# Kernel optimization log

Measured on AMD Instinct MI355X. Metric: run time of the kernel, lower is better.

## Reference

```python
import jax, jax.numpy as jnp
import numpy as np

B, N, NID, V, GH, PHI, RHO = 8, 256, 64, 128, 128, 256, 128
BN = B * N
EPS = 1e-5


def _layernorm(x, g, b):
    m = jnp.mean(x, axis=-1, keepdims=True)
    v = jnp.var(x, axis=-1, keepdims=True)
    return (x - m) * jax.lax.rsqrt(v + EPS) * g + b


def _edges(A):
    # dense adjacency -> flat batched edge list, exactly as mask.nonzero() ordering
    bidx = jnp.arange(B)[:, None, None]
    ii = jnp.arange(N)[None, :, None]
    jj = jnp.arange(N)[None, None, :]
    src = jnp.broadcast_to(bidx * N + ii, (B, N, N)).reshape(-1)  # edge_index[0] = b*N+i
    tgt = jnp.broadcast_to(bidx * N + jj, (B, N, N)).reshape(-1)  # edge_index[1] = b*N+j
    w = A.reshape(-1)
    valid = w != 0
    rel = (w > 0).astype(jnp.int32)
    return src, tgt, w, valid, rel


def _rgcn(H, src, tgt, valid, rel, Wrel, Wroot, bias):
    # torch_geometric RGCNConv: mean aggregation per relation at target + root + bias
    x_src = H[src]  # (E, d) gather
    out = H @ Wroot + bias
    for r in range(2):
        m = (valid & (rel == r)).astype(H.dtype)  # (E,)
        s = jax.ops.segment_sum(x_src * m[:, None], tgt, num_segments=BN)
        c = jax.ops.segment_sum(m, tgt, num_segments=BN)
        out = out + (s / jnp.maximum(c, 1.0)[:, None]) @ Wrel[r]
    return out


def setup_inputs() -> dict:
    key = jax.random.key(0)
    ks = jax.random.split(key, 24)
    p = lambda k, shape: jax.random.normal(k, shape, dtype=jnp.float32) * 0.02
    z = lambda *shape: jnp.zeros(shape, jnp.float32)
    return {
        "A": jax.random.normal(ks[0], (B, N, N), dtype=jnp.float32),
        "X": jax.random.normal(ks[1], (B, N, NID), dtype=jnp.float32),
        "home_mask": (jax.random.uniform(ks[2], (B, N)) > 0.5).astype(jnp.float32),
        "emb1_w": p(ks[3], (NID, V)), "emb1_b": z(V),
        "emb2_w": p(ks[4], (V, V)), "emb2_b": z(V),
        "rgcn_w_0": p(ks[5], (2, V, GH)), "rgcn_root_0": p(ks[6], (V, GH)), "rgcn_bias_0": z(GH),
        "lina_w_0": p(ks[7], (GH, GH)), "lina_b_0": z(GH),
        "linb_w_0": p(ks[8], (GH, GH)), "linb_b_0": z(GH),
        "rgcn_w_1": p(ks[9], (2, GH, GH)), "rgcn_root_1": p(ks[10], (GH, GH)), "rgcn_bias_1": z(GH),
        "lina_w_1": p(ks[11], (GH, GH)), "lina_b_1": z(GH),
        "linb_w_1": p(ks[12], (GH, GH)), "linb_b_1": z(GH),
        "norm_g": jnp.ones((GH,), jnp.float32), "norm_b": z(GH),
        "phi_w1": p(ks[13], (GH, PHI)), "phi_b1": z(PHI),
        "phi_w2": p(ks[14], (PHI, PHI)), "phi_b2": z(PHI),
        "rho_w1": p(ks[15], (PHI, RHO)), "rho_b1": z(RHO),
        "rho_w2": p(ks[16], (RHO, 1)), "rho_b2": z(1),
    }


def reference(A, X, home_mask, emb1_w, emb1_b, emb2_w, emb2_b,
              rgcn_w_0, rgcn_root_0, rgcn_bias_0, lina_w_0, lina_b_0, linb_w_0, linb_b_0,
              rgcn_w_1, rgcn_root_1, rgcn_bias_1, lina_w_1, lina_b_1, linb_w_1, linb_b_1,
              norm_g, norm_b, phi_w1, phi_b1, phi_w2, phi_b2,
              rho_w1, rho_b1, rho_w2, rho_b2):
    away_mask = 1.0 - home_mask
    H = jax.nn.relu(X @ emb1_w + emb1_b)
    H = (H @ emb2_w + emb2_b).reshape(BN, V)

    src, tgt, w, valid, rel = _edges(A)
    aw = jnp.abs(w) * valid.astype(w.dtype)  # |edge_weight|, zero for masked-out edges

    blocks = [
        (rgcn_w_0, rgcn_root_0, rgcn_bias_0, lina_w_0, lina_b_0, linb_w_0, linb_b_0),
        (rgcn_w_1, rgcn_root_1, rgcn_bias_1, lina_w_1, lina_b_1, linb_w_1, linb_b_1),
    ]
    agg = jnp.zeros_like(H)
    for (Wrel, Wroot, bias, law, lab, lbw, lbb) in blocks:
        H = H + agg
        H2 = _rgcn(H, src, tgt, valid, rel, Wrel, Wroot, bias)
        # gather-scale-scatter: agg[src] += H2[tgt] * |w|
        agg = jax.ops.segment_sum(H2[tgt] * aw[:, None], src, num_segments=BN)
        agg = jax.nn.relu(_layernorm(agg, norm_g, norm_b))  # dropout = identity (eval)
        agg = jax.nn.relu(agg @ law + lab)
        agg = agg @ lbw + lbb
    H = (H + agg).reshape(B, N, GH)

    # DeepSet phi (dropout = identity)
    h = jax.nn.relu(H @ phi_w1 + phi_b1)
    phi_out = jax.nn.relu(h @ phi_w2 + phi_b2)  # (B, N, PHI)

    home_sum = jnp.sum(phi_out * home_mask[:, :, None], axis=1)
    away_sum = jnp.sum(phi_out * away_mask[:, :, None], axis=1)

    def rho(s):
        return (jax.nn.relu(s @ rho_w1 + rho_b1) @ rho_w2 + rho_b2)[:, 0]

    out = rho(home_sum) - rho(away_sum)
    return 0.5 + 0.5 * jnp.tanh(out)  # (B,)
```

## Files before the change

kernel.cpp:

```cpp
#include <hip/hip_runtime.h>
#include <math.h>

#define NB 8

__global__ __launch_bounds__(512, 4) void k_embed(const float* __restrict__ X,
        const float* __restrict__ w1, const float* __restrict__ b1,
        const float* __restrict__ w2, const float* __restrict__ b2,
        float* __restrict__ H, float* __restrict__ pools) {
    const int r0 = blockIdx.x * 4;
    const int t = threadIdx.x, q = t & 31, u = t >> 5;
    __shared__ __align__(16) float part[8192];
    __shared__ __align__(16) float xq[256];
    __shared__ __align__(16) float h1q[512];
    if (blockIdx.x < 8) pools[blockIdx.x * 512 + t] = 0.f;
    if (t < 64) {
        float4 v;
        v.x = X[(size_t)(r0 + 0) * 64 + t];
        v.y = X[(size_t)(r0 + 1) * 64 + t];
        v.z = X[(size_t)(r0 + 2) * 64 + t];
        v.w = X[(size_t)(r0 + 3) * 64 + t];
        *(float4*)&xq[t * 4] = v;
    }
    __syncthreads();
    {
        float acc[16];
        #pragma unroll
        for (int i = 0; i < 16; ++i) acc[i] = 0.f;
        #pragma unroll
        for (int kk = 0; kk < 4; ++kk) {
            int k = u * 4 + kk;
            float4 w4 = *(const float4*)&w1[(size_t)k * 128 + q * 4];
            float wc[4] = {w4.x, w4.y, w4.z, w4.w};
            float4 x4 = *(const float4*)&xq[k * 4];
            float xr[4] = {x4.x, x4.y, x4.z, x4.w};
            #pragma unroll
            for (int r = 0; r < 4; ++r)
                #pragma unroll
                for (int c = 0; c < 4; ++c)
                    acc[r * 4 + c] = fmaf(xr[r], wc[c], acc[r * 4 + c]);
        }
        #pragma unroll
        for (int r = 0; r < 4; ++r)
            *(float4*)&part[u * 512 + r * 128 + q * 4] =
                make_float4(acc[r*4+0], acc[r*4+1], acc[r*4+2], acc[r*4+3]);
    }
    __syncthreads();
    {
        int r = t >> 7, f = t & 127;
        float s = b1[f];
        #pragma unroll
        for (int uu = 0; uu < 16; ++uu) s += part[uu * 512 + r * 128 + f];
        h1q[f * 4 + r] = fmaxf(s, 0.f);
    }
    __syncthreads();
    {
        float a2[16];
        #pragma unroll
        for (int i = 0; i < 16; ++i) a2[i] = 0.f;
        #pragma unroll
        for (int kk = 0; kk < 8; ++kk) {
            int k = u * 8 + kk;
            float4 w4 = *(const float4*)&w2[(size_t)k * 128 + q * 4];
            float wc[4] = {w4.x, w4.y, w4.z, w4.w};
            float4 h4 = *(const float4*)&h1q[k * 4];
            float hr[4] = {h4.x, h4.y, h4.z, h4.w};
            #pragma unroll
            for (int r = 0; r < 4; ++r)
                #pragma unroll
                for (int c = 0; c < 4; ++c)
                    a2[r * 4 + c] = fmaf(hr[r], wc[c], a2[r * 4 + c]);
        }
        #pragma unroll
        for (int r = 0; r < 4; ++r)
            *(float4*)&part[u * 512 + r * 128 + q * 4] =
                make_float4(a2[r*4+0], a2[r*4+1], a2[r*4+2], a2[r*4+3]);
    }
    __syncthreads();
    {
        int r = t >> 7, f = t & 127;
        float s = b2[f];
        #pragma unroll
        for (int uu = 0; uu < 16; ++uu) s += part[uu * 512 + r * 128 + f];
        H[(size_t)(r0 + r) * 128 + f] = s;
    }
}

__global__ __launch_bounds__(512, 4) void k_gcn1(
        const float* __restrict__ A, const float* __restrict__ H,
        const float* __restrict__ Wrel, const float* __restrict__ Wroot,
        const float* __restrict__ bias, float* __restrict__ H2) {
    const int b  = blockIdx.x >> 6;
    const int j0 = (blockIdx.x & 63) * 4;
    const int t = threadIdx.x, q = t & 31, u = t >> 5;
    __shared__ __align__(16) float maskM[2048];
    __shared__ __align__(16) float part[8192];
    __shared__ __align__(16) float pb[1536];
    __shared__ float cntp[256];
    __shared__ float cnt[8];
    const float* Ab = A + (size_t)b * 65536;
    const float* Hb = H + (size_t)b * 32768;
    const float* W0 = Wrel;
    const float* W1 = Wrel + 16384;

    if (t < 256) {
        float4 a = *(const float4*)(Ab + (size_t)t * 256 + j0);
        float4 m0, m1;
        m0.x = (a.x < 0.f) ? 1.f : 0.f; m1.x = (a.x > 0.f) ? 1.f : 0.f;
        m0.y = (a.y < 0.f) ? 1.f : 0.f; m1.y = (a.y > 0.f) ? 1.f : 0.f;
        m0.z = (a.z < 0.f) ? 1.f : 0.f; m1.z = (a.z > 0.f) ? 1.f : 0.f;
        m0.w = (a.w < 0.f) ? 1.f : 0.f; m1.w = (a.w > 0.f) ? 1.f : 0.f;
        *(float4*)&maskM[t * 8]     = m0;
        *(float4*)&maskM[t * 8 + 4] = m1;
    }
    __syncthreads();
    if (t < 256) {
        int chunk = t >> 3, slot = t & 7;
        float c = 0.f;
        #pragma unroll
        for (int qq = 0; qq < 8; ++qq) c += maskM[(chunk * 8 + qq) * 8 + slot];
        cntp[slot * 32 + chunk] = c;
    }
    float acc0[16], acc1[16];
    #pragma unroll
    for (int i = 0; i < 16; ++i) { acc0[i] = 0.f; acc1[i] = 0.f; }
    #pragma unroll 8
    for (int ii = 0; ii < 16; ++ii) {
        int i = u * 16 + ii;
        float4 h4 = *(const float4*)&Hb[(size_t)i * 128 + q * 4];
        float hc[4] = {h4.x, h4.y, h4.z, h4.w};
        float4 m0 = *(const float4*)&maskM[i * 8];
        float4 m1 = *(const float4*)&maskM[i * 8 + 4];
        float mr0[4] = {m0.x, m0.y, m0.z, m0.w};
        float mr1[4] = {m1.x, m1.y, m1.z, m1.w};
        #pragma unroll
        for (int r = 0; r < 4; ++r)
            #pragma unroll
            for (int c = 0; c < 4; ++c) {
                acc0[r * 4 + c] = fmaf(mr0[r], hc[c], acc0[r * 4 + c]);
                acc1[r * 4 + c] = fmaf(mr1[r], hc[c], acc1[r * 4 + c]);
            }
    }
    #pragma unroll
    for (int r = 0; r < 4; ++r)
        *(float4*)&part[u * 512 + r * 128 + q * 4] =
            make_float4(acc0[r*4+0], acc0[r*4+1], acc0[r*4+2], acc0[r*4+3]);
    if (t < 8) {
        float s = 0.f;
        #pragma unroll
        for (int c = 0; c < 32; ++c) s += cntp[t * 32 + c];
        cnt[t] = s;
    }
    __syncthreads();
    {
        int r = t >> 7, f = t & 127;
        float s = 0.f;
        #pragma unroll
        for (int uu = 0; uu < 16; ++uu) s += part[uu * 512 + r * 128 + f];
        pb[f * 12 + 4 + r] = s * (1.f / fmaxf(cnt[r], 1.f));
    }
    __syncthreads();
    #pragma unroll
    for (int r = 0; r < 4; ++r)
        *(float4*)&part[u * 512 + r * 128 + q * 4] =
            make_float4(acc1[r*4+0], acc1[r*4+1], acc1[r*4+2], acc1[r*4+3]);
    __syncthreads();
    {
        int r = t >> 7, f = t & 127;
        float s = 0.f;
        #pragma unroll
        for (int uu = 0; uu < 16; ++uu) s += part[uu * 512 + r * 128 + f];
        pb[f * 12 + 8 + r] = s * (1.f / fmaxf(cnt[4 + r], 1.f));
    }
    if (t < 128) {
        int r = t >> 5, fq = t & 31;
        float4 g4 = *(const float4*)(Hb + (size_t)(j0 + r) * 128 + fq * 4);
        pb[(fq * 4 + 0) * 12 + r] = g4.x;
        pb[(fq * 4 + 1) * 12 + r] = g4.y;
        pb[(fq * 4 + 2) * 12 + r] = g4.z;
        pb[(fq * 4 + 3) * 12 + r] = g4.w;
    }
    __syncthreads();
    float bcc[16];
    #pragma unroll
    for (int i = 0; i < 16; ++i) bcc[i] = 0.f;
    #pragma unroll 4
    for (int kk = 0; kk < 8; ++kk) {
        int k = u * 8 + kk;
        float4 wr = *(const float4*)&Wroot[(size_t)k * 128 + q * 4];
        float4 wa = *(const float4*)&W0[(size_t)k * 128 + q * 4];
        float4 wb = *(const float4*)&W1[(size_t)k * 128 + q * 4];
        float wrc[4] = {wr.x, wr.y, wr.z, wr.w};
        float wac[4] = {wa.x, wa.y, wa.z, wa.w};
        float wbc[4] = {wb.x, wb.y, wb.z, wb.w};
        float4 hv = *(const float4*)&pb[k * 12];
        float4 q0 = *(const float4*)&pb[k * 12 + 4];
        float4 q1 = *(const float4*)&pb[k * 12 + 8];
        float hr[4] = {hv.x, hv.y, hv.z, hv.w};
        float m0r[4] = {q0.x, q0.y, q0.z, q0.w};
        float m1r[4] = {q1.x, q1.y, q1.z, q1.w};
        #pragma unroll
        for (int r = 0; r < 4; ++r)
            #pragma unroll
            for (int c = 0; c < 4; ++c) {
                float v = bcc[r * 4 + c];
                v = fmaf(hr[r], wrc[c], v);
                v = fmaf(m0r[r], wac[c], v);
                v = fmaf(m1r[r], wbc[c], v);
                bcc[r * 4 + c] = v;
            }
    }
    #pragma unroll
    for (int r = 0; r < 4; ++r)
        *(float4*)&part[u * 512 + r * 128 + q * 4] =
            make_float4(bcc[r*4+0], bcc[r*4+1], bcc[r*4+2], bcc[r*4+3]);
    __syncthreads();
    {
        int r = t >> 7, f = t & 127;
        float s = bias[f];
        #pragma unroll
        for (int uu = 0; uu < 16; ++uu) s += part[uu * 512 + r * 128 + f];
        H2[(size_t)(b * 256 + j0 + r) * 128 + f] = s;
    }
}

__global__ __launch_bounds__(512, 4) void k_gcn2(
        const float* __restrict__ A, const float* __restrict__ H2,
        const float* __restrict__ g, const float* __restrict__ bta,
        const float* __restrict__ law, const float* __restrict__ lab,
        const float* __restrict__ lbw, const float* __restrict__ lbb,
        float* __restrict__ H) {
    const int b  = blockIdx.x >> 6;
    const int i0 = (blockIdx.x & 63) * 4;
    const int t = threadIdx.x, q = t & 31, u = t >> 5;
    __shared__ __align__(16) float part[8192];
    __shared__ __align__(16) float absA[1024];
    __shared__ __align__(16) float xq[512];
    __shared__ __align__(16) float uq[512];
    __shared__ float red[16];
    __shared__ float mi[8];
    const float* Ab  = A + (size_t)b * 65536;
    const float* H2b = H2 + (size_t)b * 32768;

    if (t < 256) {
        float4 av;
        av.x = fabsf(Ab[(size_t)(i0 + 0) * 256 + t]);
        av.y = fabsf(Ab[(size_t)(i0 + 1) * 256 + t]);
        av.z = fabsf(Ab[(size_t)(i0 + 2) * 256 + t]);
        av.w = fabsf(Ab[(size_t)(i0 + 3) * 256 + t]);
        *(float4*)&absA[t * 4] = av;
    }
    __syncthreads();
    float acc[16];
    #pragma unroll
    for (int i = 0; i < 16; ++i) acc[i] = 0.f;
    #pragma unroll 8
    for (int jj = 0; jj < 16; ++jj) {
        int j = u * 16 + jj;
        float4 h4 = *(const float4*)&H2b[(size_t)j * 128 + q * 4];
        float hc[4] = {h4.x, h4.y, h4.z, h4.w};
        float4 a4 = *(const float4*)&absA[j * 4];
        float ar[4] = {a4.x, a4.y, a4.z, a4.w};
        #pragma unroll
        for (int r = 0; r < 4; ++r)
            #pragma unroll
            for (int c = 0; c < 4; ++c)
                acc[r * 4 + c] = fmaf(ar[r], hc[c], acc[r * 4 + c]);
    }
    #pragma unroll
    for (int r = 0; r < 4; ++r)
        *(float4*)&part[u * 512 + r * 128 + q * 4] =
            make_float4(acc[r*4+0], acc[r*4+1], acc[r*4+2], acc[r*4+3]);
    __syncthreads();
    const int rr = t >> 7, ff = t & 127;
    float x;
    {
        float s = 0.f;
        #pragma unroll
        for (int uu = 0; uu < 16; ++uu) s += part[uu * 512 + rr * 128 + ff];
        x = s;
        float s2 = x * x;
        float sw = x;
        #pragma unroll
        for (int o = 32; o > 0; o >>= 1) {
            sw += __shfl_down(sw, o, 64);
            s2 += __shfl_down(s2, o, 64);
        }
        int w = (t >> 6) & 1;
        if ((t & 63) == 0) {
            red[(rr * 2 + w) * 2]     = sw;
            red[(rr * 2 + w) * 2 + 1] = s2;
        }
    }
    __syncthreads();
    if (t < 4) {
        float s  = red[t * 4]     + red[t * 4 + 2];
        float s2 = red[t * 4 + 1] + red[t * 4 + 3];
        float m = s * (1.f / 128.f);
        float v = s2 * (1.f / 128.f) - m * m;
        mi[t * 2] = m;
        mi[t * 2 + 1] = rsqrtf(v + 1e-5f);
    }
    __syncthreads();
    xq[ff * 4 + rr] = fmaxf((x - mi[rr * 2]) * mi[rr * 2 + 1] * g[ff] + bta[ff], 0.f);
    __syncthreads();
    float u1[16];
    #pragma unroll
    for (int i = 0; i < 16; ++i) u1[i] = 0.f;
    #pragma unroll
    for (int kk = 0; kk < 8; ++kk) {
        int k = u * 8 + kk;
        float4 w4 = *(const float4*)&law[(size_t)k * 128 + q * 4];
        float wc[4] = {w4.x, w4.y, w4.z, w4.w};
        float4 x4 = *(const float4*)&xq[k * 4];
        float xr[4] = {x4.x, x4.y, x4.z, x4.w};
        #pragma unroll
        for (int r = 0; r < 4; ++r)
            #pragma unroll
            for (int c = 0; c < 4; ++c)
                u1[r * 4 + c] = fmaf(xr[r], wc[c], u1[r * 4 + c]);
    }
    #pragma unroll
    for (int r = 0; r < 4; ++r)
        *(float4*)&part[u * 512 + r * 128 + q * 4] =
            make_float4(u1[r*4+0], u1[r*4+1], u1[r*4+2], u1[r*4+3]);
    __syncthreads();
    {
        float s = lab[ff];
        #pragma unroll
        for (int uu = 0; uu < 16; ++uu) s += part[uu * 512 + rr * 128 + ff];
        uq[ff * 4 + rr] = fmaxf(s, 0.f);
    }
    __syncthreads();
    float u2[16];
    #pragma unroll
    for (int i = 0; i < 16; ++i) u2[i] = 0.f;
    #pragma unroll
    for (int kk = 0; kk < 8; ++kk) {
        int k = u * 8 + kk;
        float4 w4 = *(const float4*)&lbw[(size_t)k * 128 + q * 4];
        float wc[4] = {w4.x, w4.y, w4.z, w4.w};
        float4 x4 = *(const float4*)&uq[k * 4];
        float xr[4] = {x4.x, x4.y, x4.z, x4.w};
        #pragma unroll
        for (int r = 0; r < 4; ++r)
            #pragma unroll
            for (int c = 0; c < 4; ++c)
                u2[r * 4 + c] = fmaf(xr[r], wc[c], u2[r * 4 + c]);
    }
    #pragma unroll
    for (int r = 0; r < 4; ++r)
        *(float4*)&part[u * 512 + r * 128 + q * 4] =
            make_float4(u2[r*4+0], u2[r*4+1], u2[r*4+2], u2[r*4+3]);
    __syncthreads();
    {
        float s = lbb[ff];
        #pragma unroll
        for (int uu = 0; uu < 16; ++uu) s += part[uu * 512 + rr * 128 + ff];
        size_t idx = (size_t)(b * 256 + i0 + rr) * 128 + ff;
        H[idx] = s + H[idx];
    }
}

__global__ __launch_bounds__(512, 4) void k_deepset(
        const float* __restrict__ H, const float* __restrict__ hm,
        const float* __restrict__ w1, const float* __restrict__ b1,
        const float* __restrict__ w2, const float* __restrict__ b2,
        float* __restrict__ hsum, float* __restrict__ asum) {
    const int r0 = blockIdx.x * 4;
    const int b  = blockIdx.x >> 6;
    const int t  = threadIdx.x, q = t & 63, u = t >> 6;
    __shared__ __align__(16) float part[8192];
    __shared__ __align__(16) float ph2[1024];
    __shared__ __align__(16) float hraw[512];
    __shared__ float hmv[4];
    if (t < 128) {
        float4 g4 = *(const float4*)&H[(size_t)r0 * 128 + t * 4];
        *(float4*)&hraw[t * 4] = g4;
    }
    if (t < 4) hmv[t] = hm[r0 + t];
    __syncthreads();
    float acc[16];
    #pragma unroll
    for (int i = 0; i < 16; ++i) acc[i] = 0.f;
    #pragma unroll 8
    for (int kk = 0; kk < 16; ++kk) {
        int k = u * 16 + kk;
        float4 w4 = *(const float4*)&w1[(size_t)k * 256 + q * 4];
        float wc[4] = {w4.x, w4.y, w4.z, w4.w};
        float hr[4];
        #pragma unroll
        for (int r = 0; r < 4; ++r) hr[r] = hraw[r * 128 + k];
        #pragma unroll
        for (int r = 0; r < 4; ++r)
            #pragma unroll
            for (int c = 0; c < 4; ++c)
                acc[r * 4 + c] = fmaf(hr[r], wc[c], acc[r * 4 + c]);
    }
    #pragma unroll
    for (int r = 0; r < 4; ++r)
        *(float4*)&part[u * 1024 + r * 256 + q * 4] =
            make_float4(acc[r*4+0], acc[r*4+1], acc[r*4+2], acc[r*4+3]);
    __syncthreads();
    {
        #pragma unroll
        for (int e = 0; e < 2; ++e) {
            int idx = e * 512 + t;
            int r = idx >> 8, f = idx & 255;
            float s = b1[f];
            #pragma unroll
            for (int uu = 0; uu < 8; ++uu) s += part[uu * 1024 + r * 256 + f];
            ph2[r * 256 + f] = fmaxf(s, 0.f);
        }
    }
    __syncthreads();
    float a2[16];
    #pragma unroll
    for (int i = 0; i < 16; ++i) a2[i] = 0.f;
    #pragma unroll 8
    for (int kk = 0; kk < 32; ++kk) {
        int k = u * 32 + kk;
        float4 w4 = *(const float4*)&w2[(size_t)k * 256 + q * 4];
        float wc[4] = {w4.x, w4.y, w4.z, w4.w};
        float pr[4];
        #pragma unroll
        for (int r = 0; r < 4; ++r) pr[r] = ph2[r * 256 + k];
        #pragma unroll
        for (int r = 0; r < 4; ++r)
            #pragma unroll
            for (int c = 0; c < 4; ++c)
                a2[r * 4 + c] = fmaf(pr[r], wc[c], a2[r * 4 + c]);
    }
    #pragma unroll
    for (int r = 0; r < 4; ++r)
        *(float4*)&part[u * 1024 + r * 256 + q * 4] =
            make_float4(a2[r*4+0], a2[r*4+1], a2[r*4+2], a2[r*4+3]);
    __syncthreads();
    if (t < 256) {
        float bb = b2[t];
        float hp = 0.f, sp = 0.f;
        #pragma unroll
        for (int r = 0; r < 4; ++r) {
            float s = bb;
            #pragma unroll
            for (int uu = 0; uu < 8; ++uu) s += part[uu * 1024 + r * 256 + t];
            float p = fmaxf(s, 0.f);
            sp += p;
            hp = fmaf(p, hmv[r], hp);
        }
        atomicAdd(&hsum[b * 256 + t], hp);
        atomicAdd(&asum[b * 256 + t], sp - hp);
    }
}

__global__ __launch_bounds__(256) void k_rho(const float* __restrict__ hsum,
        const float* __restrict__ asum,
        const float* __restrict__ w1, const float* __restrict__ b1,
        const float* __restrict__ w2, const float* __restrict__ b2,
        float* __restrict__ out) {
    const int bIdx = blockIdx.x;
    const int t = threadIdx.x, q = t & 31, u = t >> 5;
    __shared__ __align__(16) float part[2048];
    __shared__ __align__(16) float sv[512];
    __shared__ float wsv[2];
    sv[t] = hsum[bIdx * 256 + t];
    sv[256 + t] = asum[bIdx * 256 + t];
    __syncthreads();
    float aH[4] = {0.f, 0.f, 0.f, 0.f}, aA[4] = {0.f, 0.f, 0.f, 0.f};
    #pragma unroll 8
    for (int kk = 0; kk < 32; ++kk) {
        int k = u * 32 + kk;
        float4 w4 = *(const float4*)&w1[(size_t)k * 128 + q * 4];
        float sh = sv[k], sa = sv[256 + k];
        aH[0] = fmaf(sh, w4.x, aH[0]); aA[0] = fmaf(sa, w4.x, aA[0]);
        aH[1] = fmaf(sh, w4.y, aH[1]); aA[1] = fmaf(sa, w4.y, aA[1]);
        aH[2] = fmaf(sh, w4.z, aH[2]); aA[2] = fmaf(sa, w4.z, aA[2]);
        aH[3] = fmaf(sh, w4.w, aH[3]); aA[3] = fmaf(sa, w4.w, aA[3]);
    }
    *(float4*)&part[u * 256 + q * 4]       = make_float4(aH[0], aH[1], aH[2], aH[3]);
// ... 26 lines not shown
                              hipStream_t stream) {
    const float* A         = (const float*)d_in[0];
    const float* X         = (const float*)d_in[1];
    const float* home_mask = (const float*)d_in[2];
    const float* emb1_w    = (const float*)d_in[3];
    const float* emb1_b    = (const float*)d_in[4];
    const float* emb2_w    = (const float*)d_in[5];
    const float* emb2_b    = (const float*)d_in[6];
    const float* rgcn_w[2]    = { (const float*)d_in[7],  (const float*)d_in[14] };
    const float* rgcn_root[2] = { (const float*)d_in[8],  (const float*)d_in[15] };
    const float* rgcn_bias[2] = { (const float*)d_in[9],  (const float*)d_in[16] };
    const float* lina_w[2]    = { (const float*)d_in[10], (const float*)d_in[17] };
    const float* lina_b[2]    = { (const float*)d_in[11], (const float*)d_in[18] };
    const float* linb_w[2]    = { (const float*)d_in[12], (const float*)d_in[19] };
    const float* linb_b[2]    = { (const float*)d_in[13], (const float*)d_in[20] };
    const float* norm_g  = (const float*)d_in[21];
    const float* norm_b  = (const float*)d_in[22];
    const float* phi_w1  = (const float*)d_in[23];
    const float* phi_b1  = (const float*)d_in[24];
    const float* phi_w2  = (const float*)d_in[25];
    const float* phi_b2  = (const float*)d_in[26];
    const float* rho_w1  = (const float*)d_in[27];
    const float* rho_b1  = (const float*)d_in[28];
    const float* rho_w2  = (const float*)d_in[29];
    const float* rho_b2  = (const float*)d_in[30];
    float* out = (float*)d_out;

    float* ws   = (float*)d_ws;
    float* H    = ws;
    float* H2   = ws + 262144;
    float* hsum = ws + 524288;
    float* asum = ws + 526336;

    k_embed<<<512, 512, 0, stream>>>(X, emb1_w, emb1_b, emb2_w, emb2_b, H, hsum);

    for (int it = 0; it < 2; ++it) {
        k_gcn1<<<512, 512, 0, stream>>>(A, H, rgcn_w[it], rgcn_root[it],
                                        rgcn_bias[it], H2);
        k_gcn2<<<512, 512, 0, stream>>>(A, H2, norm_g, norm_b,
                                        lina_w[it], lina_b[it],
                                        linb_w[it], linb_b[it], H);
    }

    k_deepset<<<512, 512, 0, stream>>>(H, home_mask, phi_w1, phi_b1,
                                       phi_w2, phi_b2, hsum, asum);
    k_rho<<<NB, 256, 0, stream>>>(hsum, asum, rho_w1, rho_b1, rho_w2, rho_b2, out);
}
```

Before: 189.3 us.

## Process eight rows per block and pre-reduce partials with wave shuffles

Each block of the embed, GCN and DeepSet kernels now handles 8 output rows instead of 4, so every weight and H row loaded from global memory is reused across twice as many rows and the grids shrink from 512 to 256 blocks. Before each shared-memory reduction, the two half-waves of each 64-lane wave are combined with __shfl_down, so the shared partial buffer holds 8 slices instead of 16 and the final summation loop is shorter. The larger register tile (32 accumulators) and lower launch-bounds occupancy hint raise register pressure. With only 256 blocks the GPU may be underfilled, and the DeepSet kernel needs extra reduction passes and barriers.

Measured after the change: 206.5 us. +9.1%, slower.

```diff
diff --git a/kernel.cpp b/kernel.cpp
--- a/kernel.cpp
+++ b/kernel.cpp
@@ -3,296 +3,342 @@
 
 #define NB 8
 
-__global__ __launch_bounds__(512, 4) void k_embed(const float* __restrict__ X,
+
+__global__ __launch_bounds__(512, 2) void k_embed(const float* __restrict__ X,
         const float* __restrict__ w1, const float* __restrict__ b1,
         const float* __restrict__ w2, const float* __restrict__ b2,
         float* __restrict__ H, float* __restrict__ pools) {
-    const int r0 = blockIdx.x * 4;
-    const int t = threadIdx.x, q = t & 31, u = t >> 5;
+    const int r0 = blockIdx.x * 8;
+    const int t = threadIdx.x, q = t & 31, u = t >> 5, w = t >> 6;
     __shared__ __align__(16) float part[8192];
-    __shared__ __align__(16) float xq[256];
-    __shared__ __align__(16) float h1q[512];
+    __shared__ __align__(16) float xq[512];
+    __shared__ __align__(16) float h1q[1024];
     if (blockIdx.x < 8) pools[blockIdx.x * 512 + t] = 0.f;
-    if (t < 64) {
-        float4 v;
-        v.x = X[(size_t)(r0 + 0) * 64 + t];
-        v.y = X[(size_t)(r0 + 1) * 64 + t];
-        v.z = X[(size_t)(r0 + 2) * 64 + t];
-        v.w = X[(size_t)(r0 + 3) * 64 + t];
-        *(float4*)&xq[t * 4] = v;
-    }
-    __syncthreads();
-    {
-        float acc[16];
-        #pragma unroll
-        for (int i = 0; i < 16; ++i) acc[i] = 0.f;
+    {
+        int r = t >> 6, k = t & 63;
+        xq[k * 8 + r] = X[(size_t)(r0 + r) * 64 + k];
+    }
+    __syncthreads();
+    {
+        float acc[32];
+        #pragma unroll
+        for (int i = 0; i < 32; ++i) acc[i] = 0.f;
         #pragma unroll
         for (int kk = 0; kk < 4; ++kk) {
             int k = u * 4 + kk;
             float4 w4 = *(const float4*)&w1[(size_t)k * 128 + q * 4];
             float wc[4] = {w4.x, w4.y, w4.z, w4.w};
-            float4 x4 = *(const float4*)&xq[k * 4];
-            float xr[4] = {x4.x, x4.y, x4.z, x4.w};
-            #pragma unroll
-            for (int r = 0; r < 4; ++r)
+            float4 xa = *(const float4*)&xq[k * 8];
+            float4 xb = *(const float4*)&xq[k * 8 + 4];
+            float xr[8] = {xa.x, xa.y, xa.z, xa.w, xb.x, xb.y, xb.z, xb.w};
+            #pragma unroll
+            for (int r = 0; r < 8; ++r)
                 #pragma unroll
                 for (int c = 0; c < 4; ++c)
                     acc[r * 4 + c] = fmaf(xr[r], wc[c], acc[r * 4 + c]);
         }
         #pragma unroll
-        for (int r = 0; r < 4; ++r)
-            *(float4*)&part[u * 512 + r * 128 + q * 4] =
-                make_float4(acc[r*4+0], acc[r*4+1], acc[r*4+2], acc[r*4+3]);
-    }
-    __syncthreads();
-    {
-        int r = t >> 7, f = t & 127;
+        for (int i = 0; i < 32; ++i) acc[i] += __shfl_down(acc[i], 32, 64);
+        if ((t & 63) < 32)
+            #pragma unroll
+            for (int r = 0; r < 8; ++r)
+                *(float4*)&part[w * 1024 + r * 128 + q * 4] =
+                    make_float4(acc[r*4+0], acc[r*4+1], acc[r*4+2], acc[r*4+3]);
+    }
+    __syncthreads();
+    #pragma unroll
+    for (int e = 0; e < 2; ++e) {
+        int idx = e * 512 + t;
+        int r = idx >> 7, f = idx & 127;
         float s = b1[f];
         #pragma unroll
-        for (int uu = 0; uu < 16; ++uu) s += part[uu * 512 + r * 128 + f];
-        h1q[f * 4 + r] = fmaxf(s, 0.f);
-    }
-    __syncthreads();
-    {
-        float a2[16];
-        #pragma unroll
-        for (int i = 0; i < 16; ++i) a2[i] = 0.f;
+        for (int uu = 0; uu < 8; ++uu) s += part[uu * 1024 + r * 128 + f];
+        h1q[f * 8 + r] = fmaxf(s, 0.f);
+    }
+    __syncthreads();
+    {
+        float acc[32];
+        #pragma unroll
+        for (int i = 0; i < 32; ++i) acc[i] = 0.f;
         #pragma unroll
         for (int kk = 0; kk < 8; ++kk) {
             int k = u * 8 + kk;
             float4 w4 = *(const float4*)&w2[(size_t)k * 128 + q * 4];
             float wc[4] = {w4.x, w4.y, w4.z, w4.w};
-            float4 h4 = *(const float4*)&h1q[k * 4];
-            float hr[4] = {h4.x, h4.y, h4.z, h4.w};
-            #pragma unroll
-            for (int r = 0; r < 4; ++r)
+            float4 xa = *(const float4*)&h1q[k * 8];
+            float4 xb = *(const float4*)&h1q[k * 8 + 4];
+            float xr[8] = {xa.x, xa.y, xa.z, xa.w, xb.x, xb.y, xb.z, xb.w};
+            #pragma unroll
+            for (int r = 0; r < 8; ++r)
                 #pragma unroll
                 for (int c = 0; c < 4; ++c)
-                    a2[r * 4 + c] = fmaf(hr[r], wc[c], a2[r * 4 + c]);
-        }
-        #pragma unroll
-        for (int r = 0; r < 4; ++r)
-            *(float4*)&part[u * 512 + r * 128 + q * 4] =
-                make_float4(a2[r*4+0], a2[r*4+1], a2[r*4+2], a2[r*4+3]);
-    }
-    __syncthreads();
-    {
-        int r = t >> 7, f = t & 127;
+                    acc[r * 4 + c] = fmaf(xr[r], wc[c], acc[r * 4 + c]);
+        }
+        #pragma unroll
+        for (int i = 0; i < 32; ++i) acc[i] += __shfl_down(acc[i], 32, 64);
+        if ((t & 63) < 32)
+            #pragma unroll
+            for (int r = 0; r < 8; ++r)
+                *(float4*)&part[w * 1024 + r * 128 + q * 4] =
+                    make_float4(acc[r*4+0], acc[r*4+1], acc[r*4+2], acc[r*4+3]);
+    }
+    __syncthreads();
+    #pragma unroll
+    for (int e = 0; e < 2; ++e) {
+        int idx = e * 512 + t;
+        int r = idx >> 7, f = idx & 127;
         float s = b2[f];
         #pragma unroll
-        for (int uu = 0; uu < 16; ++uu) s += part[uu * 512 + r * 128 + f];
+        for (int uu = 0; uu < 8; ++uu) s += part[uu * 1024 + r * 128 + f];
         H[(size_t)(r0 + r) * 128 + f] = s;
     }
 }
 
-__global__ __launch_bounds__(512, 4) void k_gcn1(
+__global__ __launch_bounds__(512, 2) void k_gcn1(
         const float* __restrict__ A, const float* __restrict__ H,
         const float* __restrict__ Wrel, const float* __restrict__ Wroot,
         const float* __restrict__ bias, float* __restrict__ H2) {
-    const int b  = blockIdx.x >> 6;
-    const int j0 = (blockIdx.x & 63) * 4;
-    const int t = threadIdx.x, q = t & 31, u = t >> 5;
-    __shared__ __align__(16) float maskM[2048];
+    const int b  = blockIdx.x >> 5;
+    const int j0 = (blockIdx.x & 31) * 8;
+    const int t = threadIdx.x, q = t & 31, u = t >> 5, w = t >> 6;
+    __shared__ __align__(16) float maskM[4096];
     __shared__ __align__(16) float part[8192];
-    __shared__ __align__(16) float pb[1536];
-    __shared__ float cntp[256];
-    __shared__ float cnt[8];
+    __shared__ __align__(16) float pb[3072];
+    __shared__ float cntp[512];
+    __shared__ float cnt[16];
     const float* Ab = A + (size_t)b * 65536;
     const float* Hb = H + (size_t)b * 32768;
     const float* W0 = Wrel;
     const float* W1 = Wrel + 16384;
 
     if (t < 256) {
-        float4 a = *(const float4*)(Ab + (size_t)t * 256 + j0);
-        float4 m0, m1;
-        m0.x = (a.x < 0.f) ? 1.f : 0.f; m1.x = (a.x > 0.f) ? 1.f : 0.f;
-        m0.y = (a.y < 0.f) ? 1.f : 0.f; m1.y = (a.y > 0.f) ? 1.f : 0.f;
-        m0.z = (a.z < 0.f) ? 1.f : 0.f; m1.z = (a.z > 0.f) ? 1.f : 0.f;
-        m0.w = (a.w < 0.f) ? 1.f : 0.f; m1.w = (a.w > 0.f) ? 1.f : 0.f;
-        *(float4*)&maskM[t * 8]     = m0;
-        *(float4*)&maskM[t * 8 + 4] = m1;
-    }
-    __syncthreads();
-    if (t < 256) {
-        int chunk = t >> 3, slot = t & 7;
+        float4 a0 = *(const float4*)(Ab + (size_t)t * 256 + j0);
+        float4 a1 = *(const float4*)(Ab + (size_t)t * 256 + j0 + 4);
+        float av[8] = {a0.x, a0.y, a0.z, a0.w, a1.x, a1.y, a1.z, a1.w};
+        #pragma unroll
+        for (int j = 0; j < 8; ++j) {
+            maskM[t * 16 + j]     = (av[j] < 0.f) ? 1.f : 0.f;
+            maskM[t * 16 + 8 + j] = (av[j] > 0.f) ? 1.f : 0.f;
+        }
+    }
+    __syncthreads();
+    {
+        int chunk = t >> 4, slot = t & 15;
         float c = 0.f;
         #pragma unroll
-        for (int qq = 0; qq < 8; ++qq) c += maskM[(chunk * 8 + qq) * 8 + slot];
+        for (int qq = 0; qq < 8; ++qq) c += maskM[(chunk * 8 + qq) * 16 + slot];
         cntp[slot * 32 + chunk] = c;
     }
-    float acc0[16], acc1[16];
-    #pragma unroll
-    for (int i = 0; i < 16; ++i) { acc0[i] = 0.f; acc1[i] = 0.f; }
-    #pragma unroll 8
-    for (int ii = 0; ii < 16; ++ii) {
-        int i = u * 16 + ii;
-        float4 h4 = *(const float4*)&Hb[(size_t)i * 128 + q * 4];
-        float hc[4] = {h4.x, h4.y, h4.z, h4.w};
-        float4 m0 = *(const float4*)&maskM[i * 8];
-        float4 m1 = *(const float4*)&maskM[i * 8 + 4];
-        float mr0[4] = {m0.x, m0.y, m0.z, m0.w};
-        float mr1[4] = {m1.x, m1.y, m1.z, m1.w};
-        #pragma unroll
-        for (int r = 0; r < 4; ++r)
-            #pragma unroll
-            for (int c = 0; c < 4; ++c) {
-                acc0[r * 4 + c] = fmaf(mr0[r], hc[c], acc0[r * 4 + c]);
-                acc1[r * 4 + c] = fmaf(mr1[r], hc[c], acc1[r * 4 + c]);
-            }
-    }
-    #pragma unroll
-    for (int r = 0; r < 4; ++r)
-        *(float4*)&part[u * 512 + r * 128 + q * 4] =
-            make_float4(acc0[r*4+0], acc0[r*4+1], acc0[r*4+2], acc0[r*4+3]);
-    if (t < 8) {
+    __syncthreads();
+    if (t < 16) {
         float s = 0.f;
         #pragma unroll
         for (int c = 0; c < 32; ++c) s += cntp[t * 32 + c];
         cnt[t] = s;
     }
-    __syncthreads();
-    {
-        int r = t >> 7, f = t & 127;
+    {
+        float acc[32];
+        #pragma unroll
+        for (int i = 0; i < 32; ++i) acc[i] = 0.f;
+        #pragma unroll 8
+        for (int ii = 0; ii < 16; ++ii) {
+            int i = u * 16 + ii;
+            float4 h4 = *(const float4*)&Hb[(size_t)i * 128 + q * 4];
+            float hc[4] = {h4.x, h4.y, h4.z, h4.w};
+            float4 ma = *(const float4*)&maskM[i * 16];
+            float4 mb = *(const float4*)&maskM[i * 16 + 4];
+            float mr[8] = {ma.x, ma.y, ma.z, ma.w, mb.x, mb.y, mb.z, mb.w};
+            #pragma unroll
+            for (int r = 0; r < 8; ++r)
+                #pragma unroll
+                for (int c = 0; c < 4; ++c)
+                    acc[r * 4 + c] = fmaf(mr[r], hc[c], acc[r * 4 + c]);
+        }
+        #pragma unroll
+        for (int i = 0; i < 32; ++i) acc[i] += __shfl_down(acc[i], 32, 64);
+        if ((t & 63) < 32)
+            #pragma unroll
+            for (int r = 0; r < 8; ++r)
+                *(float4*)&part[w * 1024 + r * 128 + q * 4] =
+                    make_float4(acc[r*4+0], acc[r*4+1], acc[r*4+2], acc[r*4+3]);
+    }
+    __syncthreads();
+    #pragma unroll
+    for (int e = 0; e < 2; ++e) {
+        int idx = e * 512 + t;
+        int r = idx >> 7, f = idx & 127;
         float s = 0.f;
         #pragma unroll
-        for (int uu = 0; uu < 16; ++uu) s += part[uu * 512 + r * 128 + f];
-        pb[f * 12 + 4 + r] = s * (1.f / fmaxf(cnt[r], 1.f));
-    }
-    __syncthreads();
-    #pragma unroll
-    for (int r = 0; r < 4; ++r)
-        *(float4*)&part[u * 512 + r * 128 + q * 4] =
-            make_float4(acc1[r*4+0], acc1[r*4+1], acc1[r*4+2], acc1[r*4+3]);
-    __syncthreads();
-    {
-        int r = t >> 7, f = t & 127;
+        for (int uu = 0; uu < 8; ++uu) s += part[uu * 1024 + r * 128 + f];
+        pb[f * 24 + 8 + r] = s * (1.f / fmaxf(cnt[r], 1.f));
+    }
+    __syncthreads();
+    {
+        float acc[32];
+        #pragma unroll
+        for (int i = 0; i < 32; ++i) acc[i] = 0.f;
+        #pragma unroll 8
+        for (int ii = 0; ii < 16; ++ii) {
+            int i = u * 16 + ii;
+            float4 h4 = *(const float4*)&Hb[(size_t)i * 128 + q * 4];
+            float hc[4] = {h4.x, h4.y, h4.z, h4.w};
+            float4 ma = *(const float4*)&maskM[i * 16 + 8];
+            float4 mb = *(const float4*)&maskM[i * 16 + 12];
+            float mr[8] = {ma.x, ma.y, ma.z, ma.w, mb.x, mb.y, mb.z, mb.w};
+            #pragma unroll
+            for (int r = 0; r < 8; ++r)
+                #pragma unroll
+                for (int c = 0; c < 4; ++c)
+                    acc[r * 4 + c] = fmaf(mr[r], hc[c], acc[r * 4 + c]);
+        }
+        #pragma unroll
+        for (int i = 0; i < 32; ++i) acc[i] += __shfl_down(acc[i], 32, 64);
+        if ((t & 63) < 32)
+            #pragma unroll
+            for (int r = 0; r < 8; ++r)
+                *(float4*)&part[w * 1024 + r * 128 + q * 4] =
+                    make_float4(acc[r*4+0], acc[r*4+1], acc[r*4+2], acc[r*4+3]);
+    }
+    __syncthreads();
+    #pragma unroll
+    for (int e = 0; e < 2; ++e) {
+        int idx = e * 512 + t;
+        int r = idx >> 7, f = idx & 127;
         float s = 0.f;
         #pragma unroll
-        for (int uu = 0; uu < 16; ++uu) s += part[uu * 512 + r * 128 + f];
-        pb[f * 12 + 8 + r] = s * (1.f / fmaxf(cnt[4 + r], 1.f));
-    }
-    if (t < 128) {
-        int r = t >> 5, fq = t & 31;
-        float4 g4 = *(const float4*)(Hb + (size_t)(j0 + r) * 128 + fq * 4);
-        pb[(fq * 4 + 0) * 12 + r] = g4.x;
-        pb[(fq * 4 + 1) * 12 + r] = g4.y;
-        pb[(fq * 4 + 2) * 12 + r] = g4.z;
-        pb[(fq * 4 + 3) * 12 + r] = g4.w;
-    }
-    __syncthreads();
-    float bcc[16];
-    #pragma unroll
-    for (int i = 0; i < 16; ++i) bcc[i] = 0.f;
-    #pragma unroll 4
-    for (int kk = 0; kk < 8; ++kk) {
-        int k = u * 8 + kk;
-        float4 wr = *(const float4*)&Wroot[(size_t)k * 128 + q * 4];
-        float4 wa = *(const float4*)&W0[(size_t)k * 128 + q * 4];
-        float4 wb = *(const float4*)&W1[(size_t)k * 128 + q * 4];
-        float wrc[4] = {wr.x, wr.y, wr.z, wr.w};
-        float wac[4] = {wa.x, wa.y, wa.z, wa.w};
-        float wbc[4] = {wb.x, wb.y, wb.z, wb.w};
-        float4 hv = *(const float4*)&pb[k * 12];
-        float4 q0 = *(const float4*)&pb[k * 12 + 4];
-        float4 q1 = *(const float4*)&pb[k * 12 + 8];
-        float hr[4] = {hv.x, hv.y, hv.z, hv.w};
-        float m0r[4] = {q0.x, q0.y, q0.z, q0.w};
-        float m1r[4] = {q1.x, q1.y, q1.z, q1.w};
-        #pragma unroll
-        for (int r = 0; r < 4; ++r)
-            #pragma unroll
-            for (int c = 0; c < 4; ++c) {
-                float v = bcc[r * 4 + c];
-                v = fmaf(hr[r], wrc[c], v);
-                v = fmaf(m0r[r], wac[c], v);
-                v = fmaf(m1r[r], wbc[c], v);
-                bcc[r * 4 + c] = v;
-            }
-    }
-    #pragma unroll
-    for (int r = 0; r < 4; ++r)
-        *(float4*)&part[u * 512 + r * 128 + q * 4] =
-            make_float4(bcc[r*4+0], bcc[r*4+1], bcc[r*4+2], bcc[r*4+3]);
-    __syncthreads();
-    {
-        int r = t >> 7, f = t & 127;
+        for (int uu = 0; uu < 8; ++uu) s += part[uu * 1024 + r * 128 + f];
+        pb[f * 24 + 16 + r] = s * (1.f / fmaxf(cnt[8 + r], 1.f));
+        pb[f * 24 + r] = Hb[(size_t)(j0 + r) * 128 + f];
+    }
+    __syncthreads();
+    {
+        float acc[32];
+        #pragma unroll
+        for (int i = 0; i < 32; ++i) acc[i] = 0.f;
+        #pragma unroll 4
+        for (int kk = 0; kk < 8; ++kk) {
+            int k = u * 8 + kk;
+            float4 wr = *(const float4*)&Wroot[(size_t)k * 128 + q * 4];
+            float4 wa = *(const float4*)&W0[(size_t)k * 128 + q * 4];
+            float4 wb = *(const float4*)&W1[(size_t)k * 128 + q * 4];
+            float wrc[4] = {wr.x, wr.y, wr.z, wr.w};
+            float wac[4] = {wa.x, wa.y, wa.z, wa.w};
+            float wbc[4] = {wb.x, wb.y, wb.z, wb.w};
+            float4 h0 = *(const float4*)&pb[k * 24];
+            float4 h1 = *(const float4*)&pb[k * 24 + 4];
+            float4 p0 = *(const float4*)&pb[k * 24 + 8];
+            float4 p1 = *(const float4*)&pb[k * 24 + 12];
+            float4 q0 = *(const float4*)&pb[k * 24 + 16];
+            float4 q1 = *(const float4*)&pb[k * 24 + 20];
+            float hr[8]  = {h0.x, h0.y, h0.z, h0.w, h1.x, h1.y, h1.z, h1.w};
+            float m0r[8] = {p0.x, p0.y, p0.z, p0.w, p1.x, p1.y, p1.z, p1.w};
+            float m1r[8] = {q0.x, q0.y, q0.z, q0.w, q1.x, q1.y, q1.z, q1.w};
+            #pragma unroll
+            for (int r = 0; r < 8; ++r)
+                #pragma unroll
+                for (int c = 0; c < 4; ++c) {
+                    float v = acc[r * 4 + c];
+                    v = fmaf(hr[r],  wrc[c], v);
+                    v = fmaf(m0r[r], wac[c], v);
+                    v = fmaf(m1r[r], wbc[c], v);
+                    acc[r * 4 + c] = v;
+                }
+        }
+        #pragma unroll
+        for (int i = 0; i < 32; ++i) acc[i] += __shfl_down(acc[i], 32, 64);
+        if ((t & 63) < 32)
+            #pragma unroll
+            for (int r = 0; r < 8; ++r)
+                *(float4*)&part[w * 1024 + r * 128 + q * 4] =
+                    make_float4(acc[r*4+0], acc[r*4+1], acc[r*4+2], acc[r*4+3]);
+    }
+    __syncthreads();
+    #pragma unroll
+    for (int e = 0; e < 2; ++e) {
+        int idx = e * 512 + t;
+        int r = idx >> 7, f = idx & 127;
         float s = bias[f];
         #pragma unroll
-        for (int uu = 0; uu < 16; ++uu) s += part[uu * 512 + r * 128 + f];
+        for (int uu = 0; uu < 8; ++uu) s += part[uu * 1024 + r * 128 + f];
         H2[(size_t)(b * 256 + j0 + r) * 128 + f] = s;
     }
 }
 
-__global__ __launch_bounds__(512, 4) void k_gcn2(
+__global__ __launch_bounds__(512, 2) void k_gcn2(
         const float* __restrict__ A, const float* __restrict__ H2,
         const float* __restrict__ g, const float* __restrict__ bta,
         const float* __restrict__ law, const float* __restrict__ lab,
         const float* __restrict__ lbw, const float* __restrict__ lbb,
         float* __restrict__ H) {
-    const int b  = blockIdx.x >> 6;
-    const int i0 = (blockIdx.x & 63) * 4;
-    const int t = threadIdx.x, q = t & 31, u = t >> 5;
+    const int b  = blockIdx.x >> 5;
+    const int i0 = (blockIdx.x & 31) * 8;
+    const int t = threadIdx.x, q = t & 31, u = t >> 5, w = t >> 6;
     __shared__ __align__(16) float part[8192];
-    __shared__ __align__(16) float absA[1024];
-    __shared__ __align__(16) float xq[512];
-    __shared__ __align__(16) float uq[512];
-    __shared__ float red[16];
-    __shared__ float mi[8];
+    __shared__ __align__(16) float absA[2048];
+    __shared__ __align__(16) float xq[1024];
+    __shared__ __align__(16) float uq[1024];
+    __shared__ float red[32];
+    __shared__ float mi[16];
     const float* Ab  = A + (size_t)b * 65536;
     const float* H2b = H2 + (size_t)b * 32768;
 
     if (t < 256) {
-        float4 av;
-        av.x = fabsf(Ab[(size_t)(i0 + 0) * 256 + t]);
-        av.y = fabsf(Ab[(size_t)(i0 + 1) * 256 + t]);
-        av.z = fabsf(Ab[(size_t)(i0 + 2) * 256 + t]);
-        av.w = fabsf(Ab[(size_t)(i0 + 3) * 256 + t]);
-        *(float4*)&absA[t * 4] = av;
-    }
-    __syncthreads();
-    float acc[16];
-    #pragma unroll
-    for (int i = 0; i < 16; ++i) acc[i] = 0.f;
-    #pragma unroll 8
-    for (int jj = 0; jj < 16; ++jj) {
-        int j = u * 16 + jj;
-        float4 h4 = *(const float4*)&H2b[(size_t)j * 128 + q * 4];
-        float hc[4] = {h4.x, h4.y, h4.z, h4.w};
-        float4 a4 = *(const float4*)&absA[j * 4];
-        float ar[4] = {a4.x, a4.y, a4.z, a4.w};
-        #pragma unroll
-        for (int r = 0; r < 4; ++r)
-            #pragma unroll
-            for (int c = 0; c < 4; ++c)
-                acc[r * 4 + c] = fmaf(ar[r], hc[c], acc[r * 4 + c]);
-    }
-    #pragma unroll
-    for (int r = 0; r < 4; ++r)
-        *(float4*)&part[u * 512 + r * 128 + q * 4] =
-            make_float4(acc[r*4+0], acc[r*4+1], acc[r*4+2], acc[r*4+3]);
-    __syncthreads();
-    const int rr = t >> 7, ff = t & 127;
-    float x;
-    {
+        #pragma unroll
+        for (int r = 0; r < 8; ++r)
+            absA[t * 8 + r] = fabsf(Ab[(size_t)(i0 + r) * 256 + t]);
+    }
+    __syncthreads();
+    {
+        float acc[32];
+        #pragma unroll
+        for (int i = 0; i < 32; ++i) acc[i] = 0.f;
+        #pragma unroll 8
+        for (int jj = 0; jj < 16; ++jj) {
+            int j = u * 16 + jj;
+            float4 h4 = *(const float4*)&H2b[(size_t)j * 128 + q * 4];
+            float hc[4] = {h4.x, h4.y, h4.z, h4.w};
+            float4 aa = *(const float4*)&absA[j * 8];
+            float4 ab = *(const float4*)&absA[j * 8 + 4];
+            float ar[8] = {aa.x, aa.y, aa.z, aa.w, ab.x, ab.y, ab.z, ab.w};
+            #pragma unroll
+            for (int r = 0; r < 8; ++r)
+                #pragma unroll
+                for (int c = 0; c < 4; ++c)
+                    acc[r * 4 + c] = fmaf(ar[r], hc[c], acc[r * 4 + c]);
+        }
+        #pragma unroll
+        for (int i = 0; i < 32; ++i) acc[i] += __shfl_down(acc[i], 32, 64);
+        if ((t & 63) < 32)
+            #pragma unroll
+            for (int r = 0; r < 8; ++r)
+                *(float4*)&part[w * 1024 + r * 128 + q * 4] =
+                    make_float4(acc[r*4+0], acc[r*4+1], acc[r*4+2], acc[r*4+3]);
+    }
+    __syncthreads();
+    float xv[2];
+    const int fof = t & 127;
+    #pragma unroll
+    for (int e = 0; e < 2; ++e) {
+        int idx = e * 512 + t;
+        int r = idx >> 7;
         float s = 0.f;
         #pragma unroll
-        for (int uu = 0; uu < 16; ++uu) s += part[uu * 512 + rr * 128 + ff];
-        x = s;
-        float s2 = x * x;
-        float sw = x;
+        for (int uu = 0; uu < 8; ++uu) s += part[uu * 1024 + r * 128 + fof];
+        xv[e] = s;
+        float sw = s, s2 = s * s;
         #pragma unroll
         for (int o = 32; o > 0; o >>= 1) {
             sw += __shfl_down(sw, o, 64);
             s2 += __shfl_down(s2, o, 64);
         }
-        int w = (t >> 6) & 1;
         if ((t & 63) == 0) {
-            red[(rr * 2 + w) * 2]     = sw;
-            red[(rr * 2 + w) * 2 + 1] = s2;
-        }
-    }
-    __syncthreads();
-    if (t < 4) {
+            int half = (t >> 6) & 1;
+            red[r * 4 + half * 2]     = sw;
+            red[r * 4 + half * 2 + 1] = s2;
+        }
+    }
+    __syncthreads();
+    if (t < 8) {
         float s  = red[t * 4]     + red[t * 4 + 2];
         float s2 = red[t * 4 + 1] + red[t * 4 + 3];
         float m = s * (1.f / 128.f);
@@ -301,107 +347,136 @@
         mi[t * 2 + 1] = rsqrtf(v + 1e-5f);
     }
     __syncthreads();
-    xq[ff * 4 + rr] = fmaxf((x - mi[rr * 2]) * mi[rr * 2 + 1] * g[ff] + bta[ff], 0.f);
-    __syncthreads();
-    float u1[16];
-    #pragma unroll
-    for (int i = 0; i < 16; ++i) u1[i] = 0.f;
-    #pragma unroll
-    for (int kk = 0; kk < 8; ++kk) {
-        int k = u * 8 + kk;
-        float4 w4 = *(const float4*)&law[(size_t)k * 128 + q * 4];
-        float wc[4] = {w4.x, w4.y, w4.z, w4.w};
-        float4 x4 = *(const float4*)&xq[k * 4];
-        float xr[4] = {x4.x, x4.y, x4.z, x4.w};
-        #pragma unroll
-        for (int r = 0; r < 4; ++r)
-            #pragma unroll
-            for (int c = 0; c < 4; ++c)
-                u1[r * 4 + c] = fmaf(xr[r], wc[c], u1[r * 4 + c]);
-    }
-    #pragma unroll
-    for (int r = 0; r < 4; ++r)
-        *(float4*)&part[u * 512 + r * 128 + q * 4] =
-            make_float4(u1[r*4+0], u1[r*4+1], u1[r*4+2], u1[r*4+3]);
-    __syncthreads();
-    {
-        float s = lab[ff];
-        #pragma unroll
-        for (int uu = 0; uu < 16; ++uu) s += part[uu * 512 + rr * 128 + ff];
-        uq[ff * 4 + rr] = fmaxf(s, 0.f);
-    }
-    __syncthreads();
-    float u2[16];
-    #pragma unroll
-    for (int i = 0; i < 16; ++i) u2[i] = 0.f;
-    #pragma unroll
-    for (int kk = 0; kk < 8; ++kk) {
-        int k = u * 8 + kk;
-        float4 w4 = *(const float4*)&lbw[(size_t)k * 128 + q * 4];
-        float wc[4] = {w4.x, w4.y, w4.z, w4.w};
-        float4 x4 = *(const float4*)&uq[k * 4];
-        float xr[4] = {x4.x, x4.y, x4.z, x4.w};
-        #pragma unroll
-        for (int r = 0; r < 4; ++r)
-            #pragma unroll
-            for (int c = 0; c < 4; ++c)
-                u2[r * 4 + c] = fmaf(xr[r], wc[c], u2[r * 4 + c]);
-    }
-    #pragma unroll
-    for (int r = 0; r < 4; ++r)
-        *(float4*)&part[u * 512 + r * 128 + q * 4] =
-            make_float4(u2[r*4+0], u2[r*4+1], u2[r*4+2], u2[r*4+3]);
-    __syncthreads();
-    {
-        float s = lbb[ff];
-        #pragma unroll
-        for (int uu = 0; uu < 16; ++uu) s += part[uu * 512 + rr * 128 + ff];
-        size_t idx = (size_t)(b * 256 + i0 + rr) * 128 + ff;
-        H[idx] = s + H[idx];
+    {
+        float gf = g[fof], bf = bta[fof];
+        #pragma unroll
+        for (int e = 0; e < 2; ++e) {
+            int r = ((e * 512 + t) >> 7);
+            xq[fof * 8 + r] = fmaxf((xv[e] - mi[r * 2]) * mi[r * 2 + 1] * gf + bf, 0.f);
+        }
+    }
+    __syncthreads();
+    {
+        float acc[32];
+        #pragma unroll
+        for (int i = 0; i < 32; ++i) acc[i] = 0.f;
+        #pragma unroll
+        for (int kk = 0; kk < 8; ++kk) {
+            int k = u * 8 + kk;
+            float4 w4 = *(const float4*)&law[(size_t)k * 128 + q * 4];
+            float wc[4] = {w4.x, w4.y, w4.z, w4.w};
+            float4 xa = *(const float4*)&xq[k * 8];
+            float4 xb = *(const float4*)&xq[k * 8 + 4];
+            float xr[8] = {xa.x, xa.y, xa.z, xa.w, xb.x, xb.y, xb.z, xb.w};
+            #pragma unroll
+            for (int r = 0; r < 8; ++r)
+                #pragma unroll
+                for (int c = 0; c < 4; ++c)
+                    acc[r * 4 + c] = fmaf(xr[r], wc[c], acc[r * 4 + c]);
+        }
+        #pragma unroll
+        for (int i = 0; i < 32; ++i) acc[i] += __shfl_down(acc[i], 32, 64);
+        if ((t & 63) < 32)
+            #pragma unroll
+            for (int r = 0; r < 8; ++r)
+                *(float4*)&part[w * 1024 + r * 128 + q * 4] =
+                    make_float4(acc[r*4+0], acc[r*4+1], acc[r*4+2], acc[r*4+3]);
+    }
+    __syncthreads();
+    #pragma unroll
+    for (int e = 0; e < 2; ++e) {
+        int idx = e * 512 + t;
+        int r = idx >> 7, f = idx & 127;
+        float s = lab[f];
+        #pragma unroll
+        for (int uu = 0; uu < 8; ++uu) s += part[uu * 1024 + r * 128 + f];
+        uq[f * 8 + r] = fmaxf(s, 0.f);
+    }
+    __syncthreads();
+    {
+        float acc[32];
+        #pragma unroll
+        for (int i = 0; i < 32; ++i) acc[i] = 0.f;
+        #pragma unroll
+        for (int kk = 0; kk < 8; ++kk) {
+            int k = u * 8 + kk;
+            float4 w4 = *(const float4*)&lbw[(size_t)k * 128 + q * 4];
+            float wc[4] = {w4.x, w4.y, w4.z, w4.w};
+            float4 xa = *(const float4*)&uq[k * 8];
+            float4 xb = *(const float4*)&uq[k * 8 + 4];
+            float xr[8] = {xa.x, xa.y, xa.z, xa.w, xb.x, xb.y, xb.z, xb.w};
+            #pragma unroll
+            for (int r = 0; r < 8; ++r)
+                #pragma unroll
+                for (int c = 0; c < 4; ++c)
+                    acc[r * 4 + c] = fmaf(xr[r], wc[c], acc[r * 4 + c]);
+        }
+        #pragma unroll
+        for (int i = 0; i < 32; ++i) acc[i] += __shfl_down(acc[i], 32, 64);
+        if ((t & 63) < 32)
+            #pragma unroll
+            for (int r = 0; r < 8; ++r)
+                *(float4*)&part[w * 1024 + r * 128 + q * 4] =
+                    make_float4(acc[r*4+0], acc[r*4+1], acc[r*4+2], acc[r*4+3]);
+    }
+    __syncthreads();
+    #pragma unroll
+    for (int e = 0; e < 2; ++e) {
+        int idx = e * 512 + t;
+        int r = idx >> 7, f = idx & 127;
+        float s = lbb[f];
+        #pragma unroll
+        for (int uu = 0; uu < 8; ++uu) s += part[uu * 1024 + r * 128 + f];
+        size_t hidx = (size_t)(b * 256 + i0 + r) * 128 + f;
+        H[hidx] = s + H[hidx];
     }
 }
 
-__global__ __launch_bounds__(512, 4) void k_deepset(
+__global__ __launch_bounds__(512, 2) void k_deepset(
         const float* __restrict__ H, const float* __restrict__ hm,
         const float* __restrict__ w1, const float* __restrict__ b1,
         const float* __restrict__ w2, const float* __restrict__ b2,
         float* __restrict__ hsum, float* __restrict__ asum) {
-    const int r0 = blockIdx.x * 4;
-    const int b  = blockIdx.x >> 6;
+    const int r0 = blockIdx.x * 8;
+    const int b  = blockIdx.x >> 5;
     const int t  = threadIdx.x, q = t & 63, u = t >> 6;
     __shared__ __align__(16) float part[8192];
-    __shared__ __align__(16) float ph2[1024];
-    __shared__ __align__(16) float hraw[512];
-    __shared__ float hmv[4];
-    if (t < 128) {
-        float4 g4 = *(const float4*)&H[(size_t)r0 * 128 + t * 4];
-        *(float4*)&hraw[t * 4] = g4;
-    }
-    if (t < 4) hmv[t] = hm[r0 + t];
-    __syncthreads();
-    float acc[16];
-    #pragma unroll
-    for (int i = 0; i < 16; ++i) acc[i] = 0.f;
+    __shared__ __align__(16) float ph2[2048];
+    __shared__ __align__(16) float hraw[1024];
+    __shared__ float hmv[8];
+    #pragma unroll
+    for (int e = 0; e < 2; ++e) {
+        int idx = e * 512 + t;
+        int r = idx >> 7, k = idx & 127;
+        hraw[k * 8 + r] = H[(size_t)(r0 + r) * 128 + k];
+    }
+    if (t < 8) hmv[t] = hm[r0 + t];
+    __syncthreads();
+    float acc[32];
+    #pragma unroll
+    for (int i = 0; i < 32; ++i) acc[i] = 0.f;
     #pragma unroll 8
     for (int kk = 0; kk < 16; ++kk) {
         int k = u * 16 + kk;
         float4 w4 = *(const float4*)&w1[(size_t)k * 256 + q * 4];
         float wc[4] = {w4.x, w4.y, w4.z, w4.w};
-        float hr[4];
-        #pragma unroll
-        for (int r = 0; r < 4; ++r) hr[r] = hraw[r * 128 + k];
-        #pragma unroll
-        for (int r = 0; r < 4; ++r)
+        float4 ha = *(const float4*)&hraw[k * 8];
+        float4 hb = *(const float4*)&hraw[k * 8 + 4];
+        float hr[8] = {ha.x, ha.y, ha.z, ha.w, hb.x, hb.y, hb.z, hb.w};
+        #pragma unroll
+        for (int r = 0; r < 8; ++r)
             #pragma unroll
             for (int c = 0; c < 4; ++c)
                 acc[r * 4 + c] = fmaf(hr[r], wc[c], acc[r * 4 + c]);
     }
     #pragma unroll
-    for (int r = 0; r < 4; ++r)
-        *(float4*)&part[u * 1024 + r * 256 + q * 4] =
-            make_float4(acc[r*4+0], acc[r*4+1], acc[r*4+2], acc[r*4+3]);
-    __syncthreads();
-    {
+    for (int pass = 0; pass < 2; ++pass) {
+        #pragma unroll
+        for (int r = 0; r < 4; ++r)
+            *(float4*)&part[u * 1024 + r * 256 + q * 4] =
+                make_float4(acc[(pass*4+r)*4+0], acc[(pass*4+r)*4+1],
+                            acc[(pass*4+r)*4+2], acc[(pass*4+r)*4+3]);
+        __syncthreads();
         #pragma unroll
         for (int e = 0; e < 2; ++e) {
             int idx = e * 512 + t;
@@ -409,41 +484,53 @@
             float s = b1[f];
             #pragma unroll
             for (int uu = 0; uu < 8; ++uu) s += part[uu * 1024 + r * 256 + f];
-            ph2[r * 256 + f] = fmaxf(s, 0.f);
-        }
-    }
-    __syncthreads();
-    float a2[16];
-    #pragma unroll
-    for (int i = 0; i < 16; ++i) a2[i] = 0.f;
+            ph2[f * 8 + pass * 4 + r] = fmaxf(s, 0.f);
+        }
+        __syncthreads();
+    }
+    float a2[32];
+    #pragma unroll
+    for (int i = 0; i < 32; ++i) a2[i] = 0.f;
     #pragma unroll 8
     for (int kk = 0; kk < 32; ++kk) {
         int k = u * 32 + kk;
         float4 w4 = *(const float4*)&w2[(size_t)k * 256 + q * 4];
         float wc[4] = {w4.x, w4.y, w4.z, w4.w};
-        float pr[4];
-        #pragma unroll
-        for (int r = 0; r < 4; ++r) pr[r] = ph2[r * 256 + k];
-        #pragma unroll
-        for (int r = 0; r < 4; ++r)
+        float4 pa = *(const float4*)&ph2[k * 8];
+        float4 pbv = *(const float4*)&ph2[k * 8 + 4];
+        float pr[8] = {pa.x, pa.y, pa.z, pa.w, pbv.x, pbv.y, pbv.z, pbv.w};
+        #pragma unroll
+        for (int r = 0; r < 8; ++r)
             #pragma unroll
             for (int c = 0; c < 4; ++c)
                 a2[r * 4 + c] = fmaf(pr[r], wc[c], a2[r * 4 + c]);
     }
-    #pragma unroll
-    for (int r = 0; r < 4; ++r)
-        *(float4*)&part[u * 1024 + r * 256 + q * 4] =
-            make_float4(a2[r*4+0], a2[r*4+1], a2[r*4+2], a2[r*4+3]);
-    __syncthreads();
+    __syncthreads();
+    #pragma unroll
+    for (int pass = 0; pass < 2; ++pass) {
+        #pragma unroll
+        for (int r = 0; r < 4; ++r)
+            *(float4*)&part[u * 1024 + r * 256 + q * 4] =
+                make_float4(a2[(pass*4+r)*4+0], a2[(pass*4+r)*4+1],
+                            a2[(pass*4+r)*4+2], a2[(pass*4+r)*4+3]);
+        __syncthreads();
+        #pragma unroll
+        for (int e = 0; e < 2; ++e) {
+            int idx = e * 512 + t;
+            int r = idx >> 8, f = idx & 255;
+            float s = 0.f;
+            #pragma unroll
+            for (int uu = 0; uu < 8; ++uu) s += part[uu * 1024 + r * 256 + f];
+            ph2[f * 8 + pass * 4 + r] = s;
+        }
+        __syncthreads();
+    }
     if (t < 256) {
         float bb = b2[t];
         float hp = 0.f, sp = 0.f;
         #pragma unroll
-        for (int r = 0; r < 4; ++r) {
-            float s = bb;
-            #pragma unroll
-            for (int uu = 0; uu < 8; ++uu) s += part[uu * 1024 + r * 256 + t];
-            float p = fmaxf(s, 0.f);
+        for (int r = 0; r < 8; ++r) {
+            float p = fmaxf(ph2[t * 8 + r] + bb, 0.f);
             sp += p;
             hp = fmaf(p, hmv[r], hp);
         }
@@ -536,17 +623,17 @@
     float* hsum = ws + 524288;
     float* asum = ws + 526336;
 
-    k_embed<<<512, 512, 0, stream>>>(X, emb1_w, emb1_b, emb2_w, emb2_b, H, hsum);
+    k_embed<<<256, 512, 0, stream>>>(X, emb1_w, emb1_b, emb2_w, emb2_b, H, hsum);
 
     for (int it = 0; it < 2; ++it) {
-        k_gcn1<<<512, 512, 0, stream>>>(A, H, rgcn_w[it], rgcn_root[it],
+        k_gcn1<<<256, 512, 0, stream>>>(A, H, rgcn_w[it], rgcn_root[it],
                                         rgcn_bias[it], H2);
-        k_gcn2<<<512, 512, 0, stream>>>(A, H2, norm_g, norm_b,
+        k_gcn2<<<256, 512, 0, stream>>>(A, H2, norm_g, norm_b,
                                         lina_w[it], lina_b[it],
                                         linb_w[it], linb_b[it], H);
     }
 
-    k_deepset<<<512, 512, 0, stream>>>(H, home_mask, phi_w1, phi_b1,
+    k_deepset<<<256, 512, 0, stream>>>(H, home_mask, phi_w1, phi_b1,
                                        phi_w2, phi_b2, hsum, asum);
     k_rho<<<NB, 256, 0, stream>>>(hsum, asum, rho_w1, rho_b1, rho_w2, rho_b2, out);
 }
```
